# Optimization experiments

Hardware: AMD Instinct MI355X
Metric: run time of the kernel (lower is better)

## Reference

```python
import jax, jax.numpy as jnp
import numpy as np

B, N, D_IN, D_OUT = 4096, 200, 64, 64


def setup_inputs() -> dict:
    key = jax.random.key(0)
    k1, k2 = jax.random.split(key)
    x = jax.random.normal(k1, (B, N, D_IN), dtype=jnp.float32)
    # weight initialized like TF add_weight default (glorot-ish scale via normal here)
    weight = jax.random.normal(k2, (1, N, D_IN, D_OUT), dtype=jnp.float32) * (1.0 / np.sqrt(D_IN))
    bias = jnp.zeros((1, N, D_OUT), dtype=jnp.float32)
    return {"x": x, "weight": weight, "bias": bias}


def reference(x, weight, bias):
    # Original: (x[..., None] * weight).sum(-2) + bias
    # == per-token matmul: out[b,n,o] = sum_i x[b,n,i] * weight[0,n,i,o] + bias[0,n,o]
    out = jnp.einsum('bni,nio->bno', x, weight[0])
    return out + bias
```

## Files before the change

### kernel.cpp

```cpp
#include <hip/hip_runtime.h>


#define B_DIM 4096
#define N_DIM 200
#define D 64
#define ROWS_PER_BLOCK 256

typedef __attribute__((ext_vector_type(8))) _Float16 half8;
typedef __attribute__((ext_vector_type(4))) float f32x4;

__device__ __forceinline__ void split8(const float4 a, const float4 b,
                                       half8& h, half8& l) {
  const float f[8] = {a.x, a.y, a.z, a.w, b.x, b.y, b.z, b.w};
#pragma unroll
  for (int j = 0; j < 8; ++j) {
    const _Float16 hh = (_Float16)f[j];
    h[j] = hh;
    l[j] = (_Float16)(f[j] - (float)hh);
  }
}

__global__ __launch_bounds__(256)
void w_prep(const float* __restrict__ w,
            half8* __restrict__ wh, half8* __restrict__ wl) {
  const int n    = blockIdx.x;
  const int tid  = threadIdx.x;
  const int lane = tid & 63;
  const int g    = tid >> 6;
  const int c    = lane & 15;
  const int kg   = lane >> 4;
  const float* wn = w + (size_t)n * (D * D);
#pragma unroll
  for (int t = 0; t < 2; ++t) {
    const int combo = g * 2 + t;
    const int ks = combo >> 2;
    const int of = combo & 3;
    half8 h, l;
#pragma unroll
    for (int j = 0; j < 8; ++j) {
      const int k = ks * 32 + kg * 8 + j;
      const float v = wn[k * D + of * 16 + c];
      const _Float16 hh = (_Float16)v;
      h[j] = hh;
      l[j] = (_Float16)(v - (float)hh);
    }
    const size_t idx = ((size_t)(n * 2 + ks) * 4 + of) * 64 + lane;
    wh[idx] = h;
    wl[idx] = l;
  }
}

template <bool PREPPED>
__global__ __launch_bounds__(256, 3)
void nlinear_main(const float* __restrict__ x,
                  const float* __restrict__ w,
                  const float* __restrict__ bias,
                  const half8* __restrict__ wh,
                  const half8* __restrict__ wl,
                  float* __restrict__ out) {
  const int n    = blockIdx.y;
  const int tid  = threadIdx.x;
  const int lane = tid & 63;
  const int wave = tid >> 6;
  const int c    = lane & 15;
  const int kg   = lane >> 4;

  half8 Wh[2][4], Wl[2][4];
  if (PREPPED) {
#pragma unroll
    for (int ks = 0; ks < 2; ++ks)
#pragma unroll
      for (int of = 0; of < 4; ++of) {
        const size_t idx = ((size_t)(n * 2 + ks) * 4 + of) * 64 + lane;
        Wh[ks][of] = wh[idx];
        Wl[ks][of] = wl[idx];
      }
  } else {
    const float* wn = w + (size_t)n * (D * D);
#pragma unroll
    for (int ks = 0; ks < 2; ++ks)
#pragma unroll
      for (int of = 0; of < 4; ++of)
#pragma unroll
        for (int j = 0; j < 8; ++j) {
          const float v = wn[(ks * 32 + kg * 8 + j) * D + of * 16 + c];
          const _Float16 hh = (_Float16)v;
          Wh[ks][of][j] = hh;
          Wl[ks][of][j] = (_Float16)(v - (float)hh);
        }
  }

  float4 bv4[4];
#pragma unroll
  for (int of = 0; of < 4; ++of)
    bv4[of] = *(const float4*)(bias + (size_t)n * D + of * 16 + kg * 4);

  const size_t rstride = (size_t)N_DIM * D;
  const int row0 = blockIdx.x * ROWS_PER_BLOCK + wave * 64;
  const float* xb = x + (size_t)row0 * rstride + (size_t)n * D;
  float* ob = out + (size_t)row0 * rstride + (size_t)n * D;

  auto xaddr = [&](int mf) {
    return xb + (size_t)(mf * 16 + c) * rstride + kg * 8;
  };

  float4 P[2][4];
  {
    const float* p0 = xaddr(0);
    P[0][0] = *(const float4*)(p0);
    P[0][1] = *(const float4*)(p0 + 4);
    P[0][2] = *(const float4*)(p0 + 32);
    P[0][3] = *(const float4*)(p0 + 36);
    const float* p1 = xaddr(1);
    P[1][0] = *(const float4*)(p1);
    P[1][1] = *(const float4*)(p1 + 4);
    P[1][2] = *(const float4*)(p1 + 32);
    P[1][3] = *(const float4*)(p1 + 36);
  }

#pragma unroll
  for (int mf = 0; mf < 4; ++mf) {
    const int buf = mf & 1;
    const float4 v0 = P[buf][0], v1 = P[buf][1];
    const float4 v2 = P[buf][2], v3 = P[buf][3];
    if (mf < 2) {
      const float* pn = xaddr(mf + 2);
      P[buf][0] = *(const float4*)(pn);
      P[buf][1] = *(const float4*)(pn + 4);
      P[buf][2] = *(const float4*)(pn + 32);
      P[buf][3] = *(const float4*)(pn + 36);
    }

    half8 ah0, al0, ah1, al1;
    split8(v0, v1, ah0, al0);
    split8(v2, v3, ah1, al1);

    f32x4 acc[4];
#pragma unroll
    for (int of = 0; of < 4; ++of) {
      f32x4 t = {bv4[of].x, bv4[of].y, bv4[of].z, bv4[of].w};
      acc[of] = t;
    }

#pragma unroll
    for (int of = 0; of < 4; ++of) {
      acc[of] = __builtin_amdgcn_mfma_f32_16x16x32_f16(Wh[0][of], ah0, acc[of], 0, 0, 0);
      acc[of] = __builtin_amdgcn_mfma_f32_16x16x32_f16(Wl[0][of], ah0, acc[of], 0, 0, 0);
      acc[of] = __builtin_amdgcn_mfma_f32_16x16x32_f16(Wh[0][of], al0, acc[of], 0, 0, 0);
      acc[of] = __builtin_amdgcn_mfma_f32_16x16x32_f16(Wh[1][of], ah1, acc[of], 0, 0, 0);
      acc[of] = __builtin_amdgcn_mfma_f32_16x16x32_f16(Wl[1][of], ah1, acc[of], 0, 0, 0);
      acc[of] = __builtin_amdgcn_mfma_f32_16x16x32_f16(Wh[1][of], al1, acc[of], 0, 0, 0);
    }

    float* orow = ob + (size_t)(mf * 16 + c) * rstride;
#pragma unroll
    for (int of = 0; of < 4; ++of)
      *(f32x4*)(orow + of * 16 + kg * 4) = acc[of];
  }
}

extern "C" void kernel_launch(void* const* d_in, const int* in_sizes, int n_in,
                              void* d_out, int out_size, void* d_ws, size_t ws_size,
                              hipStream_t stream) {
  const float* x    = (const float*)d_in[0];
  const float* w    = (const float*)d_in[1];
  const float* bias = (const float*)d_in[2];
  float*       out  = (float*)d_out;

  const size_t NFRAGS = (size_t)N_DIM * 2 * 4 * 64;
  const size_t NEED   = NFRAGS * 16 * 2;

  dim3 grid(B_DIM / ROWS_PER_BLOCK, N_DIM);
  if (d_ws && ws_size >= NEED) {
    half8* whp = (half8*)d_ws;
    half8* wlp = whp + NFRAGS;
    w_prep<<<dim3(N_DIM), dim3(256), 0, stream>>>(w, whp, wlp);
    nlinear_main<true><<<grid, dim3(256), 0, stream>>>(x, w, bias, whp, wlp, out);
  } else {
    nlinear_main<false><<<grid, dim3(256), 0, stream>>>(x, w, bias, nullptr, nullptr, out);
  }
}
```

Measured before the change: 377.3 us.

## Stage x tiles through LDS with async global_load_lds and coalesced stores

Each block now covers 4 consecutive tokens (one per wave) over 64 rows. Contiguous 1KB row segments are staged into swizzled LDS with global_load_lds, double-buffered across 16-row chunks. Outputs are written back through LDS so global stores are full coalesced rows instead of strided 16B pieces. This targets poor coalescing of the per-token 256B accesses, but adds block-wide barriers and LDS traffic, and each block now reloads weights for fewer rows.

```diff
diff --git a/kernel.cpp b/kernel.cpp
--- a/kernel.cpp
+++ b/kernel.cpp
@@ -1,10 +1,14 @@
 #include <hip/hip_runtime.h>
+#include <stdint.h>
 
 
 #define B_DIM 4096
 #define N_DIM 200
 #define D 64
-#define ROWS_PER_BLOCK 256
+#define NCH 4
+#define RT 16
+#define RPB 64
+#define NCHUNK (RPB / RT)
 
 typedef __attribute__((ext_vector_type(8))) _Float16 half8;
 typedef __attribute__((ext_vector_type(4))) float f32x4;
@@ -18,6 +22,12 @@
     h[j] = hh;
     l[j] = (_Float16)(f[j] - (float)hh);
   }
+}
+
+__device__ __forceinline__ void gl16(const float* g, float* l) {
+  __builtin_amdgcn_global_load_lds(
+      (const __attribute__((address_space(1))) void*)g,
+      (__attribute__((address_space(3))) void*)l, 16, 0, 0);
 }
 
 __global__ __launch_bounds__(256)
@@ -51,19 +61,24 @@
 }
 
 template <bool PREPPED>
-__global__ __launch_bounds__(256, 3)
-void nlinear_main(const float* __restrict__ x,
-                  const float* __restrict__ w,
-                  const float* __restrict__ bias,
-                  const half8* __restrict__ wh,
-                  const half8* __restrict__ wl,
-                  float* __restrict__ out) {
-  const int n    = blockIdx.y;
+__global__ __launch_bounds__(256, 4)
+void nlinear_v5(const float* __restrict__ x,
+                const float* __restrict__ w,
+                const float* __restrict__ bias,
+                const half8* __restrict__ wh,
+                const half8* __restrict__ wl,
+                float* __restrict__ out) {
   const int tid  = threadIdx.x;
   const int lane = tid & 63;
   const int wave = tid >> 6;
   const int c    = lane & 15;
   const int kg   = lane >> 4;
+  const int nc   = blockIdx.y;
+  const int n    = nc * NCH + wave;
+  const int r0   = blockIdx.x * RPB;
+  const int sw   = c & 7;
+
+  __shared__ float xbuf[2][RT][NCH * D];
 
   half8 Wh[2][4], Wl[2][4];
   if (PREPPED) {
@@ -96,40 +111,41 @@
     bv4[of] = *(const float4*)(bias + (size_t)n * D + of * 16 + kg * 4);
 
   const size_t rstride = (size_t)N_DIM * D;
-  const int row0 = blockIdx.x * ROWS_PER_BLOCK + wave * 64;
-  const float* xb = x + (size_t)row0 * rstride + (size_t)n * D;
-  float* ob = out + (size_t)row0 * rstride + (size_t)n * D;
-
-  auto xaddr = [&](int mf) {
-    return xb + (size_t)(mf * 16 + c) * rstride + kg * 8;
+  const float* xtile = x   + (size_t)r0 * rstride + (size_t)nc * (NCH * D);
+  float*       otile = out + (size_t)r0 * rstride + (size_t)nc * (NCH * D);
+
+  auto stage = [&](int ch, int b) {
+    const float* base = xtile + (size_t)ch * RT * rstride;
+    float* lbase = &xbuf[b][0][0];
+#pragma unroll
+    for (int k = 0; k < 4; ++k) {
+      const int row = wave + 4 * k;
+      const int pp  = lane ^ (row & 7);
+      gl16(base + (size_t)row * rstride + (size_t)pp * 4,
+           lbase + (size_t)(tid + 256 * k) * 4);
+    }
   };
 
-  float4 P[2][4];
-  {
-    const float* p0 = xaddr(0);
-    P[0][0] = *(const float4*)(p0);
-    P[0][1] = *(const float4*)(p0 + 4);
-    P[0][2] = *(const float4*)(p0 + 32);
-    P[0][3] = *(const float4*)(p0 + 36);
-    const float* p1 = xaddr(1);
-    P[1][0] = *(const float4*)(p1);
-    P[1][1] = *(const float4*)(p1 + 4);
-    P[1][2] = *(const float4*)(p1 + 32);
-    P[1][3] = *(const float4*)(p1 + 36);
-  }
-
-#pragma unroll
-  for (int mf = 0; mf < 4; ++mf) {
-    const int buf = mf & 1;
-    const float4 v0 = P[buf][0], v1 = P[buf][1];
-    const float4 v2 = P[buf][2], v3 = P[buf][3];
-    if (mf < 2) {
-      const float* pn = xaddr(mf + 2);
-      P[buf][0] = *(const float4*)(pn);
-      P[buf][1] = *(const float4*)(pn + 4);
-      P[buf][2] = *(const float4*)(pn + 32);
-      P[buf][3] = *(const float4*)(pn + 36);
-    }
+  stage(0, 0);
+
+  for (int ch = 0; ch < NCHUNK; ++ch) {
+    const int cur = ch & 1;
+    if (ch + 1 < NCHUNK) {
+      stage(ch + 1, cur ^ 1);
+      asm volatile("s_waitcnt vmcnt(4)" ::: "memory");
+    } else {
+      asm volatile("s_waitcnt vmcnt(0)" ::: "memory");
+    }
+    __builtin_amdgcn_sched_barrier(0);
+    __builtin_amdgcn_s_barrier();
+    __builtin_amdgcn_sched_barrier(0);
+
+    const float4* lp = (const float4*)&xbuf[cur][0][0];
+    const int fbase = c * 64 + wave * 16 + kg * 2;
+    const float4 v0 = lp[(fbase + 0) ^ sw];
+    const float4 v1 = lp[(fbase + 1) ^ sw];
+    const float4 v2 = lp[(fbase + 8) ^ sw];
+    const float4 v3 = lp[(fbase + 9) ^ sw];
 
     half8 ah0, al0, ah1, al1;
     split8(v0, v1, ah0, al0);
@@ -141,7 +157,6 @@
       f32x4 t = {bv4[of].x, bv4[of].y, bv4[of].z, bv4[of].w};
       acc[of] = t;
     }
-
 #pragma unroll
     for (int of = 0; of < 4; ++of) {
       acc[of] = __builtin_amdgcn_mfma_f32_16x16x32_f16(Wh[0][of], ah0, acc[of], 0, 0, 0);
@@ -152,10 +167,27 @@
       acc[of] = __builtin_amdgcn_mfma_f32_16x16x32_f16(Wh[1][of], al1, acc[of], 0, 0, 0);
     }
 
-    float* orow = ob + (size_t)(mf * 16 + c) * rstride;
+    f32x4* op = (f32x4*)&xbuf[cur][0][0];
 #pragma unroll
     for (int of = 0; of < 4; ++of)
-      *(f32x4*)(orow + of * 16 + kg * 4) = acc[of];
+      op[(c * 64 + wave * 16 + of * 4 + kg) ^ sw] = acc[of];
+
+    asm volatile("s_waitcnt lgkmcnt(0)" ::: "memory");
+    __builtin_amdgcn_sched_barrier(0);
+    __builtin_amdgcn_s_barrier();
+    __builtin_amdgcn_sched_barrier(0);
+
+    const float4* rp = (const float4*)&xbuf[cur][0][0];
+#pragma unroll
+    for (int k = 0; k < 4; ++k) {
+      const int row = wave + 4 * k;
+      const float4 vv = rp[(tid + 256 * k) ^ (row & 7)];
+      *(float4*)(otile + (size_t)(ch * RT + row) * rstride + lane * 4) = vv;
+    }
+
+    __builtin_amdgcn_sched_barrier(0);
+    __builtin_amdgcn_s_barrier();
+    __builtin_amdgcn_sched_barrier(0);
   }
 }
 
@@ -170,13 +202,13 @@
   const size_t NFRAGS = (size_t)N_DIM * 2 * 4 * 64;
   const size_t NEED   = NFRAGS * 16 * 2;
 
-  dim3 grid(B_DIM / ROWS_PER_BLOCK, N_DIM);
+  dim3 grid(B_DIM / RPB, N_DIM / NCH);
   if (d_ws && ws_size >= NEED) {
     half8* whp = (half8*)d_ws;
     half8* wlp = whp + NFRAGS;
     w_prep<<<dim3(N_DIM), dim3(256), 0, stream>>>(w, whp, wlp);
-    nlinear_main<true><<<grid, dim3(256), 0, stream>>>(x, w, bias, whp, wlp, out);
+    nlinear_v5<true><<<grid, dim3(256), 0, stream>>>(x, w, bias, whp, wlp, out);
   } else {
-    nlinear_main<false><<<grid, dim3(256), 0, stream>>>(x, w, bias, nullptr, nullptr, out);
-  }
-}
+    nlinear_v5<false><<<grid, dim3(256), 0, stream>>>(x, w, bias, nullptr, nullptr, out);
+  }
+}
```

New measurement: 383.8 us. Within noise of the previous version (+1.7%).
